# Performance work log

Measured on AMD Instinct MI355X. Metric: run time of the kernel, lower is better.

## Reference

```python
import jax, jax.numpy as jnp
import numpy as np

EPS = 1e-8
TEMP = 0.1
D, H = 512, 256  # hidden_dim, hidden_dim // 2
BI, R = 64, 36   # images, regions
BC, W = 64, 50   # captions, words


def _l2norm(x):
    n = jnp.linalg.norm(x, axis=-1, keepdims=True)
    return x / jnp.maximum(n, 1e-12)


def _gate(x, w1, b1, w2, b2):
    h = jax.nn.relu(x @ w1 + b1)
    return jax.nn.sigmoid(h @ w2 + b2)  # [..., 1]


def setup_inputs() -> dict:
    key = jax.random.key(0)
    ks = jax.random.split(key, 12)
    imgs = jax.random.normal(ks[0], (BI, R, D), dtype=jnp.float32)
    caps = jax.random.normal(ks[1], (BC, W, D), dtype=jnp.float32)
    img_lens = jax.random.randint(ks[2], (BI,), 1, R + 1).at[0].set(R).astype(jnp.int32)
    cap_lens = jax.random.randint(ks[3], (BC,), 1, W + 1).at[0].set(W).astype(jnp.int32)
    s = 0.02
    return {
        'imgs': imgs, 'caps': caps,
        'soft_w1': jax.random.normal(ks[4], (D, H), dtype=jnp.float32) * s,
        'soft_b1': jnp.zeros((H,), dtype=jnp.float32),
        'soft_w2': jax.random.normal(ks[5], (H, 1), dtype=jnp.float32) * s,
        'soft_b2': jnp.zeros((1,), dtype=jnp.float32),
        'hard_w1': jax.random.normal(ks[6], (D, H), dtype=jnp.float32) * s,
        'hard_b1': jnp.zeros((H,), dtype=jnp.float32),
        'hard_w2': jax.random.normal(ks[7], (H, 1), dtype=jnp.float32) * s,
        'hard_b2': jnp.zeros((1,), dtype=jnp.float32),
        'img_lens': img_lens, 'cap_lens': cap_lens,
    }


def reference(imgs, caps, soft_w1, soft_b1, soft_w2, soft_b2,
              hard_w1, hard_b1, hard_w2, hard_b2, img_lens, cap_lens):
    Bi, R_, D_ = imgs.shape
    Bc, W_, _ = caps.shape
    img_mask = jnp.arange(R_)[None, :] < img_lens[:, None]  # [Bi,R]
    cap_mask = jnp.arange(W_)[None, :] < cap_lens[:, None]  # [Bc,W]
    mask = img_mask[:, None, :, None] & cap_mask[None, :, None, :]  # [Bi,Bc,R,W]

    # fine-grained region-word similarities
    sims = jnp.einsum('ird,cwd->icrw', imgs, caps)

    # hard (top-1) attention: argmax over words, one-hot scatter, re-masked
    idx = jnp.argmax(jnp.where(mask, sims, -1.0), axis=-1)  # [Bi,Bc,R]
    hard_attn = jnp.where(mask, jax.nn.one_hot(idx, W_, dtype=sims.dtype), 0.0)

    # soft attention with temperature and mask
    soft = jax.nn.softmax(jnp.where(mask, sims / TEMP, -jnp.inf), axis=-1)
    soft_attn = jnp.where(mask, soft, 0.0)

    hard_wc = jnp.einsum('icrw,cwd->icrd', hard_attn, caps)
    soft_wc = jnp.einsum('icrw,cwd->icrd', soft_attn, caps)

    # per-region learned gates, normalized to sum ~1
    sg = _gate(imgs, soft_w1, soft_b1, soft_w2, soft_b2)  # [Bi,R,1]
    hg = _gate(imgs, hard_w1, hard_b1, hard_w2, hard_b2)  # [Bi,R,1]
    tot = sg + hg + EPS
    sg = (sg / tot)[:, None, :, :]  # [Bi,1,R,1]
    hg = (hg / tot)[:, None, :, :]

    mixed = sg * soft_wc + hg * hard_wc  # [Bi,Bc,R,D]

    # per-pair, per-region cosine similarity
    out = jnp.einsum('ird,icrd->icr', _l2norm(imgs), _l2norm(mixed))
    return jnp.where(img_mask[:, None, :], out, -1.0)  # [Bi,Bc,R]
```

## Files before the change

kernel.cpp:

```cpp
#include <hip/hip_runtime.h>
#include <math.h>

#define BI 64
#define RR 36
#define BC 64
#define WW 50
#define DD 512
#define HH 256
#define CST 132

typedef _Float16 f16x8 __attribute__((ext_vector_type(8)));
typedef _Float16 f16x4 __attribute__((ext_vector_type(4)));
typedef float    f32x4 __attribute__((ext_vector_type(4)));
typedef float    f32x16 __attribute__((ext_vector_type(16)));

__device__ __forceinline__ float wave_sum(float v){
  #pragma unroll
  for (int off=32; off>0; off>>=1) v += __shfl_xor(v, off, 64);
  return v;
}
__device__ __forceinline__ float wave_max(float v){
  #pragma unroll
  for (int off=32; off>0; off>>=1) v = fmaxf(v, __shfl_xor(v, off, 64));
  return v;
}

__device__ __forceinline__ void gl_lds16(const _Float16* g, _Float16* l){
  __builtin_amdgcn_global_load_lds(
      (const __attribute__((address_space(1))) unsigned int*)g,
      (__attribute__((address_space(3))) unsigned int*)l, 16, 0, 0);
}

__global__ __launch_bounds__(256) void prepgram_kernel(
    const float* __restrict__ imgs, const float* __restrict__ caps,
    const float* __restrict__ sw1, const float* __restrict__ hw1,
    _Float16* __restrict__ Ah, _Float16* __restrict__ Al,
    _Float16* __restrict__ Bh, _Float16* __restrict__ Bl,
    float* __restrict__ G, _Float16* __restrict__ Gfrag)
{
  __shared__ __align__(16) float smem[64*64];
  if (blockIdx.x < 1504){
    int u = blockIdx.x*256 + threadIdx.x;
    _Float16 *dh, *dl; int idx;
    if (u < 144*1024){ idx = u;            dh = Ah; dl = Al; }
    else             { idx = u - 144*1024; dh = Bh; dl = Bl; }
    const int tile = idx >> 10, rem = idx & 1023, ks = rem >> 6, lane = rem & 63;
    const int k0 = ks*32 + (lane >> 4)*8;
    f16x8 hv, lv;
    if (u < 144*1024 || tile < 200){
      const float* src = (u < 144*1024) ? imgs : caps;
      const int m = tile*16 + (lane & 15);
      const float* p = src + (size_t)m*DD + k0;
      #pragma unroll
      for (int j=0;j<8;j++){
        float a = p[j];
        _Float16 h = (_Float16)a;
        hv[j] = h;
        lv[j] = (_Float16)((a - (float)h) * 2048.0f);
      }
    } else {
      const int n = (tile-200)*16 + (lane & 15);
      const float* src = (n < HH) ? (sw1 + n) : (hw1 + n - HH);
      #pragma unroll
      for (int j=0;j<8;j++){
        float a = src[(size_t)(k0+j)*HH];
        _Float16 h = (_Float16)a;
        hv[j] = h;
        lv[j] = (_Float16)((a - (float)h) * 2048.0f);
      }
    }
    *(f16x8*)(dh + (size_t)idx*8) = hv;
    *(f16x8*)(dl + (size_t)idx*8) = lv;
  } else {
    float* Gt = smem;
    const int c = blockIdx.x - 1504;
    const int t = threadIdx.x, lane = t & 63, wv = t >> 6;
    const int wm = wv & 1, wn = wv >> 1;
    const float* cbase = caps + (size_t)c*WW*DD;

    f32x16 P, Q;
    #pragma unroll
    for (int e=0;e<16;e++){ P[e]=0.f; Q[e]=0.f; }

    const int r  = lane & 31;
    const int k8 = (lane >> 5)*8;
    const int wA = wm*32 + r;
    const int wB = wn*32 + r;
    const float* pA = cbase + (size_t)wA*DD + k8;
    const float* pB = cbase + (size_t)wB*DD + k8;

    for (int ks=0; ks<32; ks++){
      const int k0 = ks*16;
      float4 a0, a1, b0, b1;
      if (wA < WW){ a0 = *(const float4*)(pA + k0); a1 = *(const float4*)(pA + k0 + 4); }
      else        { a0 = (float4){0,0,0,0}; a1 = a0; }
      if (wB < WW){ b0 = *(const float4*)(pB + k0); b1 = *(const float4*)(pB + k0 + 4); }
      else        { b0 = (float4){0,0,0,0}; b1 = b0; }
      float av[8] = {a0.x,a0.y,a0.z,a0.w,a1.x,a1.y,a1.z,a1.w};
      float bw[8] = {b0.x,b0.y,b0.z,b0.w,b1.x,b1.y,b1.z,b1.w};
      f16x8 ah, al, bh, bl;
      #pragma unroll
      for (int j=0;j<8;j++){
        _Float16 h = (_Float16)av[j];
        ah[j] = h; al[j] = (_Float16)((av[j]-(float)h)*2048.0f);
        _Float16 g = (_Float16)bw[j];
        bh[j] = g; bl[j] = (_Float16)((bw[j]-(float)g)*2048.0f);
      }
      P = __builtin_amdgcn_mfma_f32_32x32x16_f16(ah, bh, P,0,0,0);
      Q = __builtin_amdgcn_mfma_f32_32x32x16_f16(ah, bl, Q,0,0,0);
      Q = __builtin_amdgcn_mfma_f32_32x32x16_f16(al, bh, Q,0,0,0);
    }

    const int col = wn*32 + (lane & 31);
    #pragma unroll
    for (int reg=0; reg<16; reg++){
      const int row = wm*32 + (reg&3) + 8*(reg>>2) + 4*(lane>>5);
      float g = P[reg] + Q[reg]*(1.0f/2048.0f);
      Gt[row*64 + col] = g;
      if (row < WW && col < WW)
        G[(size_t)c*WW*WW + row*WW + col] = g;
    }
    __syncthreads();

    #pragma unroll
    for (int tile=0; tile<4; tile++){
      int flat = t*4;
      int ks2 = flat>>9, L=(flat>>3)&63, j0=flat&7;
      const bool ones = (tile==3) && ((L&15)==2);
      int n  = tile*16 + (L&15);
      int kk = ks2*32 + ((L>>4)<<3) + j0;
      f16x4 v;
      #pragma unroll
      for (int e=0;e<4;e++)
        v[e] = ones ? (_Float16)1.0f : (_Float16)Gt[n*64 + kk + e];
      *(f16x4*)&Gfrag[(size_t)c*4096 + (tile*2+ks2)*512 + L*8 + j0] = v;
    }
  }
}

__global__ __launch_bounds__(256, 2) void sgemm_hgate_kernel(
    const _Float16* __restrict__ Ah, const _Float16* __restrict__ Al,
    const _Float16* __restrict__ Bh, const _Float16* __restrict__ Bl,
    float* __restrict__ Sp,
    const float* __restrict__ imgs,
    const float* __restrict__ sb1, const float* __restrict__ hb1,
    const float* __restrict__ sw2, const float* __restrict__ hw2,
    float* __restrict__ drawS, float* __restrict__ drawH,
    float* __restrict__ rnraw)
{
  __shared__ _Float16 lds[2*16384];
  const int t = threadIdx.x, lane = t & 63, wv = t >> 6;

  if (blockIdx.x >= 36){
    const int sg  = blockIdx.x - 36;
    const int xcd = sg & 7, sidx = sg >> 3;
    const int l   = (xcd < 2 ? xcd*57 : 114 + (xcd-2)*56) + sidx;
    const int st  = l / 45, wi = l - st*45;
    const int mbg = st & 1, nbg = st >> 1;
    const int mb  = mbg*9 + wi/5;
    const int nb  = nbg*5 + wi%5;
    const int wm = wv & 1, wn = wv >> 1;

    f32x4 P[4][4], Q[4][4];
    #pragma unroll
    for (int a=0;a<4;a++)
      #pragma unroll
      for (int b=0;b<4;b++){ P[a][b]=(f32x4){0,0,0,0}; Q[a][b]=(f32x4){0,0,0,0}; }

    const _Float16* sbase = (wv==0)?Ah:(wv==1)?Al:(wv==2)?Bh:Bl;
    const size_t gtb = (size_t)((wv<2)? mb : nb)*8;
    _Float16* buf0 = lds + wv*4096;
    _Float16* buf1 = lds + 16384 + wv*4096;

    #pragma unroll
    for (int s=0;s<8;s++)
      gl_lds16(sbase + (((gtb+s)*16 + 0)*64 + lane)*8, buf0 + s*512);
    asm volatile("s_waitcnt vmcnt(0)" ::: "memory");
    __syncthreads();

    for (int ks=0; ks<16; ks++){
      if (ks < 15){
        _Float16* nb_ = ((ks+1) & 1) ? buf1 : buf0;
        #pragma unroll
        for (int s=0;s<8;s++)
          gl_lds16(sbase + (((gtb+s)*16 + (ks+1))*64 + lane)*8, nb_ + s*512);
      }

      const _Float16* L = lds + (ks & 1)*16384;
      f16x8 a_h[4], a_l[4], b_h[4], b_l[4];
      #pragma unroll
      for (int x=0;x<4;x++){
        a_h[x] = *(const f16x8*)&L[        (wm*4+x)*512 + lane*8];
        a_l[x] = *(const f16x8*)&L[ 4096 + (wm*4+x)*512 + lane*8];
        b_h[x] = *(const f16x8*)&L[ 8192 + (wn*4+x)*512 + lane*8];
        b_l[x] = *(const f16x8*)&L[12288 + (wn*4+x)*512 + lane*8];
      }
      #pragma unroll
      for (int mi=0;mi<4;mi++)
        #pragma unroll
        for (int ni=0;ni<4;ni++){
          P[mi][ni] = __builtin_amdgcn_mfma_f32_16x16x32_f16(a_h[mi], b_h[ni], P[mi][ni],0,0,0);
          Q[mi][ni] = __builtin_amdgcn_mfma_f32_16x16x32_f16(a_h[mi], b_l[ni], Q[mi][ni],0,0,0);
          Q[mi][ni] = __builtin_amdgcn_mfma_f32_16x16x32_f16(a_l[mi], b_h[ni], Q[mi][ni],0,0,0);
        }

      if (ks < 15)
        asm volatile("s_waitcnt vmcnt(0)" ::: "memory");
      __syncthreads();
    }

    const int r0 = mb*128 + wm*64 + ((lane>>4)<<2);
    const int c0 = nb*128 + wn*64 + (lane&15);
    size_t pr[16]; size_t pc[4];
    #pragma unroll
    for (int mi=0;mi<4;mi++)
      #pragma unroll
      for (int reg=0;reg<4;reg++){
        unsigned row = (unsigned)(r0 + mi*16 + reg);
        unsigned i = row / 36u, rr_ = row - i*36u;
        pr[mi*4+reg] = (size_t)i*115200u + (size_t)rr_*50u;
      }
    #pragma unroll
    for (int ni=0;ni<4;ni++){
      unsigned col = (unsigned)(c0 + ni*16);
      unsigned cc = col / 50u, w = col - cc*50u;
      pc[ni] = (size_t)cc*1800u + w;
    }
    #pragma unroll
    for (int mi=0;mi<4;mi++)
      #pragma unroll
      for (int ni=0;ni<4;ni++)
        #pragma unroll
        for (int reg=0;reg<4;reg++)
          Sp[pr[mi*4+reg] + pc[ni]] =
              P[mi][ni][reg] + Q[mi][ni][reg]*(1.0f/2048.0f);
    return;
  }

  const int mb = blockIdx.x >> 1;
  const int br = blockIdx.x & 1;
  const int wm = wv & 1, wn = wv >> 1;

  f32x4 P[4][8];
  #pragma unroll
  for (int a=0;a<4;a++)
    #pragma unroll
    for (int b=0;b<8;b++) P[a][b]=(f32x4){0,0,0,0};

  const _Float16* Bbase = Bh + (size_t)(200 + br*16)*8192;

  #pragma unroll
  for (int s=0;s<6;s++){
    const int u = wv*6 + s;
    const _Float16* src = (u < 8)
      ? (Ah    + ((size_t)((mb*8 + u)*16 + 0)*64 + lane)*8)
      : (Bbase + ((size_t)((u-8)  *16 + 0)*64 + lane)*8);
    _Float16* dst = (u < 8) ? (lds + u*512) : (lds + 4096 + (u-8)*512);
    gl_lds16(src, dst);
  }
  asm volatile("s_waitcnt vmcnt(0)" ::: "memory");
  __syncthreads();

  for (int ks=0; ks<16; ks++){
    if (ks < 15){
      _Float16* buf = lds + (((ks+1) & 1) ? 16384 : 0);
      #pragma unroll
      for (int s=0;s<6;s++){
        const int u = wv*6 + s;
        const _Float16* src = (u < 8)
          ? (Ah    + ((size_t)((mb*8 + u)*16 + (ks+1))*64 + lane)*8)
          : (Bbase + ((size_t)((u-8)  *16 + (ks+1))*64 + lane)*8);
        _Float16* dst = (u < 8) ? (buf + u*512) : (buf + 4096 + (u-8)*512);
        gl_lds16(src, dst);
      }
    }

    const _Float16* L = lds + (ks & 1)*16384;
    f16x8 a[4], b[8];
    #pragma unroll
    for (int x=0;x<4;x++)
      a[x] = *(const f16x8*)&L[(wm*4+x)*512 + lane*8];
    #pragma unroll
    for (int y=0;y<8;y++)
      b[y] = *(const f16x8*)&L[4096 + (wn*8+y)*512 + lane*8];
    #pragma unroll
    for (int mi=0;mi<4;mi++)
      #pragma unroll
      for (int ni=0;ni<8;ni++)
        P[mi][ni] = __builtin_amdgcn_mfma_f32_16x16x32_f16(a[mi], b[ni], P[mi][ni],0,0,0);

    if (ks < 15)
      asm volatile("s_waitcnt vmcnt(0)" ::: "memory");
    __syncthreads();
  }

  const float* b1 = br ? hb1 : sb1;
  const float* w2 = br ? hw2 : sw2;
  float bvv[8], wvv[8];
  #pragma unroll
  for (int ni=0;ni<8;ni++){
    const int cb = wn*128 + ni*16 + (lane&15);
    bvv[ni] = b1[cb]; wvv[ni] = w2[cb];
  }
  float contrib[16];
  #pragma unroll
  for (int mi=0;mi<4;mi++)
    #pragma unroll
    for (int reg=0;reg<4;reg++){
      float cacc = 0.f;
      #pragma unroll
      for (int ni=0;ni<8;ni++)
        cacc = fmaf(fmaxf(P[mi][ni][reg] + bvv[ni], 0.f), wvv[ni], cacc);
      #pragma unroll
      for (int off=1; off<16; off<<=1) cacc += __shfl_xor(cacc, off, 64);
      contrib[mi*4+reg] = cacc;
    }

  float* red = (float*)lds;
  if ((lane & 15) == 0){
    const int rbase = wm*64 + ((lane>>4)<<2);
    #pragma unroll
    for (int mi=0;mi<4;mi++)
      #pragma unroll
      for (int reg=0;reg<4;reg++)
        red[wn*128 + rbase + mi*16 + reg] = contrib[mi*4+reg];
  }
  __syncthreads();
  if (t < 128){
    float draw = red[t] + red[128 + t];
    (br ? drawH : drawS)[mb*128 + t] = draw;
  }

  if (br == 0){
    const int row = mb*128 + (t >> 1);
    const float* p = imgs + (size_t)row*DD + (t & 1)*256;
    float ss = 0.f;
    #pragma unroll
    for (int q=0;q<64;q++){
      float4 x = ((const float4*)p)[q];
      ss += x.x*x.x + x.y*x.y + x.z*x.z + x.w*x.w;
    }
    ss += __shfl_xor(ss, 1, 64);
    if ((t & 1) == 0) rnraw[row] = ss;
  }
}

__global__ __launch_bounds__(512) void epi_kernel(
    const float* __restrict__ Sp,
    const int* __restrict__ img_lens, const int* __restrict__ cap_lens,
    const float* __restrict__ drawS, const float* __restrict__ drawH,
    const float* __restrict__ rnraw,
    const float* __restrict__ G, const _Float16* __restrict__ Gfrag,
    const float* __restrict__ sb2, const float* __restrict__ hb2,
    float* __restrict__ out)
{
  __shared__ __align__(16) _Float16 sEp[48*72];
  __shared__ __align__(16) _Float16 sE2[48*72];
  __shared__ __align__(16) _Float16 sFp[48*72];
  __shared__ __align__(16) _Float16 sGf[4096];
  __shared__ float sTd[48];
  __shared__ float sTS[48];
  __shared__ float sGd[64];
  __shared__ float sAv[40];
  __shared__ int   sAi[40];

  const int bx = blockIdx.x;
  const int i = bx >> 6, c = bx & 63;
  const int t = threadIdx.x, lane = t & 63;
  const int wv = __builtin_amdgcn_readfirstlane(t >> 6);
  const int cap_len = cap_lens[c];
  const int img_len = img_lens[i];

  ((int4*)sGf)[t] = ((const int4*)(Gfrag + (size_t)c*4096))[t];
  if (t < WW) sGd[t] = G[(size_t)c*WW*WW + t*(WW+1)];

  const int r0 = wv*5;
  const float* srow = Sp + (size_t)(i*64 + c)*1800u + (size_t)r0*50;
  float sv[5];
  #pragma unroll
  for (int j=0;j<5;j++)
    sv[j] = ((r0+j) < RR && lane < WW) ? srow[j*50 + lane] : 0.f;

  #pragma unroll
  for (int j=0;j<5;j++){
    const int r = r0 + j;
    const float s = sv[j];
    const bool valid = (lane < cap_len);
    float av = wave_max(valid ? s : -INFINITY);
    unsigned long long m = __ballot(valid && (s == av));
    int ai = (int)(__ffsll((long long)m) - 1);
    float e = valid ? __expf(10.0f*(s - av)) : 0.f;
    sEp[r*72 + lane] = (_Float16)e;
    sE2[r*72 + lane] = (_Float16)(e * s);
    if (lane == 0){ sAv[r] = av; sAi[r] = ai; }
  }
  __syncthreads();

  {
    int mi = wv % 3, nt = wv / 3;
    f32x4 acc = (f32x4){0,0,0,0};
    #pragma unroll
    for (int ks=0; ks<2; ks++){
      f16x8 a = *(const f16x8*)&sEp[(mi*16+(lane&15))*72 + ks*32 + ((lane>>4)<<3)];
      f16x8 b = *(const f16x8*)&sGf[(nt*2+ks)*512 + lane*8];
      acc = __builtin_amdgcn_mfma_f32_16x16x32_f16(a, b, acc, 0,0,0);
    }
    #pragma unroll
    for (int reg=0; reg<4; reg++){
      int row = mi*16 + ((lane>>4)<<2) + reg;
      sFp[row*72 + nt*16 + (lane&15)] = (_Float16)acc[reg];
    }
  }
  if (wv < 4){
    int tau = 8 + wv, mi = tau % 3, nt = tau / 3;
    f32x4 acc = (f32x4){0,0,0,0};
    #pragma unroll
    for (int ks=0; ks<2; ks++){
      f16x8 a = *(const f16x8*)&sEp[(mi*16+(lane&15))*72 + ks*32 + ((lane>>4)<<3)];
      f16x8 b = *(const f16x8*)&sGf[(nt*2+ks)*512 + lane*8];
      acc = __builtin_amdgcn_mfma_f32_16x16x32_f16(a, b, acc, 0,0,0);
    }
    #pragma unroll
    for (int reg=0; reg<4; reg++){
      int row = mi*16 + ((lane>>4)<<2) + reg;
      sFp[row*72 + nt*16 + (lane&15)] = (_Float16)acc[reg];
    }
  } else if (wv < 7){
    int mi = wv - 4;
    f32x4 acc = (f32x4){0,0,0,0};
    #pragma unroll
    for (int ks=0; ks<2; ks++){
      f16x8 a = *(const f16x8*)&sE2[(mi*16+(lane&15))*72 + ks*32 + ((lane>>4)<<3)];
      f16x8 b = *(const f16x8*)&sGf[(3*2+ks)*512 + lane*8];
      acc = __builtin_amdgcn_mfma_f32_16x16x32_f16(a, b, acc, 0,0,0);
    }
    if ((lane & 15) == 2){
      #pragma unroll
      for (int reg=0; reg<4; reg++)
        sTS[mi*16 + ((lane>>4)<<2) + reg] = acc[reg];
    }
  }
  __syncthreads();

  if (wv < 3){
    f32x4 acc = (f32x4){0,0,0,0};
    #pragma unroll
    for (int ks=0; ks<2; ks++){
      f16x8 aF = *(const f16x8*)&sFp[(wv*16+(lane&15))*72 + ks*32 + ((lane>>4)<<3)];
      f16x8 bE = *(const f16x8*)&sEp[(wv*16+(lane&15))*72 + ks*32 + ((lane>>4)<<3)];
      acc = __builtin_amdgcn_mfma_f32_16x16x32_f16(aF, bE, acc, 0,0,0);
    }
    #pragma unroll
    for (int reg=0; reg<4; reg++){
      int row = ((lane>>4)<<2) + reg;
      if (row == (lane&15)) sTd[wv*16 + row] = acc[reg];
    }
  }
  __syncthreads();

  if (wv == 0 && lane < RR){
    const int r = lane;
    const int ai = sAi[r];
    const float av = sAv[r];
    float tQ  = sTd[r];
    float tS  = sTS[r];
    float den = (float)sFp[r*72 + 50];
    float dh  = (float)sFp[r*72 + ai];
    float hh  = sGd[ai];
    float hv  = (av > -1.0f) ? 1.f : 0.f;

    const int rg = i*RR + r;
    float sg_ = 1.f/(1.f+__expf(-(drawS[rg] + sb2[0])));
    float hg_ = 1.f/(1.f+__expf(-(drawH[rg] + hb2[0])));
    float tot = sg_ + hg_ + 1e-8f;
    float gs = sg_/tot, gh = hg_/tot;
    float rx = 1.f/fmaxf(sqrtf(rnraw[rg]), 1e-12f);
    float rd = 1.f/den;
    float num = gs*(tS*rd) + hv*gh*av;
    float n2  = gs*gs*(tQ*rd*rd) + hv*(2.f*gs*gh*(dh*rd) + gh*gh*hh);
    float ov  = num * rx / fmaxf(sqrtf(fmaxf(n2, 0.f)), 1e-12f);
    out[((size_t)i*BC + c)*RR + r] = (r < img_len) ? ov : -1.0f;
  }
}

__global__ __launch_bounds__(256) void gates_kernel(
    const float* __restrict__ imgs,
    const float* __restrict__ sw1, const float* __restrict__ sb1,
    const float* __restrict__ sw2, const float* __restrict__ sb2,
    const float* __restrict__ hw1, const float* __restrict__ hb1,
    const float* __restrict__ hw2, const float* __restrict__ hb2,
    float* __restrict__ sgn, float* __restrict__ hgn, float* __restrict__ rn)
{
  __shared__ __align__(16) float xs[8*DD];
  __shared__ float red[16*256];
  __shared__ float nr[8];
  const int t = threadIdx.x;
  const int row0 = blockIdx.x * 8;
  if (t < 8) nr[t] = 0.f;
  __syncthreads();
  const float4* src = (const float4*)(imgs + (size_t)row0*DD);
  #pragma unroll
  for (int m=0;m<4;m++){
    int n = m*256+t;
    float4 v = src[n];
    ((float4*)xs)[n] = v;
    float ss = v.x*v.x+v.y*v.y+v.z*v.z+v.w*v.w;
    atomicAdd(&nr[n>>7], ss);
  }
  __syncthreads();
  float accS[8]={0,0,0,0,0,0,0,0};
  float accH[8]={0,0,0,0,0,0,0,0};
  for (int k=0;k<DD;k+=4){
    float a0=sw1[(k+0)*HH+t], a1=sw1[(k+1)*HH+t], a2=sw1[(k+2)*HH+t], a3=sw1[(k+3)*HH+t];
    float b0=hw1[(k+0)*HH+t], b1=hw1[(k+1)*HH+t], b2=hw1[(k+2)*HH+t], b3=hw1[(k+3)*HH+t];
    #pragma unroll
    for (int r=0;r<8;r++){
      float4 x = *(const float4*)&xs[r*DD+k];
      accS[r]=fmaf(x.x,a0,accS[r]); accS[r]=fmaf(x.y,a1,accS[r]);
      accS[r]=fmaf(x.z,a2,accS[r]); accS[r]=fmaf(x.w,a3,accS[r]);
      accH[r]=fmaf(x.x,b0,accH[r]); accH[r]=fmaf(x.y,b1,accH[r]);
      accH[r]=fmaf(x.z,b2,accH[r]); accH[r]=fmaf(x.w,b3,accH[r]);
    }
  }
  const float b1s=sb1[t], b1h=hb1[t], w2s=sw2[t], w2h=hw2[t];
  #pragma unroll
  for (int r=0;r<8;r++){
    red[r*256+t]     = w2s * fmaxf(accS[r]+b1s, 0.f);
    red[(8+r)*256+t] = w2h * fmaxf(accH[r]+b1h, 0.f);
  }
  __syncthreads();
  const int wv=t>>6, ln=t&63;
  #pragma unroll
  for (int q=0;q<4;q++){
    int rr_ = wv*4+q;
    float v = red[rr_*256+ln]+red[rr_*256+ln+64]+red[rr_*256+ln+128]+red[rr_*256+ln+192];
    v = wave_sum(v);
    if (ln==0) red[rr_*256] = v;
  }
  __syncthreads();
  if (t<8){
    float os = red[t*256] + sb2[0];
    float oh = red[(8+t)*256] + hb2[0];
    float s = 1.f/(1.f+__expf(-os));
    float h = 1.f/(1.f+__expf(-oh));
    float tot = s+h+1e-8f;
    sgn[row0+t] = s/tot;
    hgn[row0+t] = h/tot;
    rn[row0+t]  = 1.f/fmaxf(sqrtf(nr[t]), 1e-12f);
  }
}

__global__ __launch_bounds__(256) void gram_fb_kernel(
    const float* __restrict__ caps, float* __restrict__ G)
{
  __shared__ __align__(16) float cs[WW*CST];
  const int c    = blockIdx.x >> 2;
  const int tile = blockIdx.x & 3;
  const int w0   = tile*13;
  const int nw   = (tile==3) ? 11 : 13;
  const int t=threadIdx.x, lane=t&63, wv=t>>6;
  const int wl = lane < WW ? lane : WW-1;
  float acc[4]={0.f,0.f,0.f,0.f};
  for (int k0=0;k0<DD;k0+=128){
    __syncthreads();
    for (int n=t;n<WW*32;n+=256){
      int row=n>>5, c4=(n&31)*4;
      *(float4*)&cs[row*CST+c4] = *(const float4*)(caps + ((size_t)c*WW+row)*DD + k0 + c4);
    }
    __syncthreads();
    for (int k=0;k<128;k+=4){
      float4 cv = *(const float4*)&cs[wl*CST+k];
      #pragma unroll
      for (int q=0;q<4;q++){
        int lw = wv + q*4;
        if (lw < nw){
          float4 bv = *(const float4*)&cs[(w0+lw)*CST+k];
          acc[q]=fmaf(bv.x,cv.x,acc[q]); acc[q]=fmaf(bv.y,cv.y,acc[q]);
          acc[q]=fmaf(bv.z,cv.z,acc[q]); acc[q]=fmaf(bv.w,cv.w,acc[q]);
        }
      }
    }
  }
  if (lane < WW){
    #pragma unroll
    for (int q=0;q<4;q++){
      int lw = wv + q*4;
      if (lw < nw) G[(size_t)c*WW*WW + (w0+lw)*WW + lane] = acc[q];
    }
  }
}

__global__ __launch_bounds__(256) void pair_kernel(
    const float* __restrict__ imgs, const float* __restrict__ caps,
    const int* __restrict__ img_lens, const int* __restrict__ cap_lens,
    const float* __restrict__ sgn, const float* __restrict__ hgn,
    const float* __restrict__ rn,
    const float* __restrict__ G, float* __restrict__ out)
{
  __shared__ __align__(16) float smem[WW*CST + 52*52 + RR*52];
  float* cs = smem;
  float* Gs = smem + WW*CST;
  float* As = Gs + 52*52;
  const int bx = blockIdx.x;
  const int i = bx >> 6, c = bx & 63;
  const int t = threadIdx.x, lane = t&63;
  const int wv = __builtin_amdgcn_readfirstlane(t>>6);
  const int wl = lane < WW ? lane : WW-1;
  const int cap_len = cap_lens[c];
  const int img_len = img_lens[i];
  for (int n=t;n<52*52;n+=256){
    int w=n/52, w2=n-w*52;
    Gs[n] = (w<WW && w2<WW) ? G[(size_t)c*WW*WW + w*WW + w2] : 0.f;
  }
  float acc[9]={0,0,0,0,0,0,0,0,0};
  const float* ib = imgs + ((size_t)i*RR + wv*9)*DD;
  for (int k0=0;k0<DD;k0+=128){
    __syncthreads();
    for (int n=t;n<WW*32;n+=256){
      int row=n>>5, c4=(n&31)*4;
      *(float4*)&cs[row*CST+c4] = *(const float4*)(caps + ((size_t)c*WW+row)*DD + k0 + c4);
    }
    __syncthreads();
    for (int k=0;k<128;k+=4){
      float4 cv = *(const float4*)&cs[wl*CST+k];
      #pragma unroll
      for (int j=0;j<9;j++){
        float4 iv = *(const float4*)(ib + j*DD + k0 + k);
        acc[j]=fmaf(iv.x,cv.x,acc[j]); acc[j]=fmaf(iv.y,cv.y,acc[j]);
        acc[j]=fmaf(iv.z,cv.z,acc[j]); acc[j]=fmaf(iv.w,cv.w,acc[j]);
      }
    }
  }
  for (int j=0;j<9;j++){
    const int r = wv*9 + j;
    const float s = acc[j];
    float av; int ai;
    if (lane < cap_len){ av = s;     ai = lane; }
    else if (lane < WW){ av = -1.0f; ai = lane; }
    else               { av = -INFINITY; ai = 64; }
    #pragma unroll
    for (int off=32; off>0; off>>=1){
      float ov = __shfl_xor(av, off, 64);
      int   oi = __shfl_xor(ai, off, 64);
      if (ov > av || (ov == av && oi < ai)){ av = ov; ai = oi; }
    }
    float zv = (lane < cap_len) ? s*10.0f : -INFINITY;
    float zm = wave_max(zv);
    float e  = (lane < cap_len) ? __expf(zv - zm) : 0.f;
    float den = wave_sum(e);
    if (lane < 52) As[r*52 + lane] = (lane < WW) ? e : 0.f;
    float m = 0.f;
    #pragma unroll
    for (int g=0; g<13; g++){
      float4 ab = *(const float4*)&As[r*52 + g*4];
      m = fmaf(ab.x, Gs[(g*4+0)*52+wl], m);
      m = fmaf(ab.y, Gs[(g*4+1)*52+wl], m);
      m = fmaf(ab.z, Gs[(g*4+2)*52+wl], m);
      m = fmaf(ab.w, Gs[(g*4+3)*52+wl], m);
    }
    float tS = wave_sum(e * s);
    float tQ = wave_sum(e * m);
    float dh = __shfl(m, ai, 64);
    float hh = Gs[ai*52 + ai];
    float hv = (ai < cap_len) ? 1.f : 0.f;
    const int rg = i*RR + r;
    float gs = sgn[rg], gh = hgn[rg], rx = rn[rg];
    float rd = 1.f/den;
    float num = gs*(tS*rd) + hv*gh*av;
    float n2  = gs*gs*(tQ*rd*rd) + hv*(2.f*gs*gh*(dh*rd) + gh*gh*hh);
    float ov  = num * rx / fmaxf(sqrtf(fmaxf(n2, 0.f)), 1e-12f);
    if (lane==0) out[((size_t)i*BC + c)*RR + r] = (r < img_len) ? ov : -1.0f;
  }
}

extern "C" void kernel_launch(void* const* d_in, const int* in_sizes, int n_in,
                              void* d_out, int out_size, void* d_ws, size_t ws_size,
                              hipStream_t stream)
{
  const float* imgs = (const float*)d_in[0];
  const float* caps = (const float*)d_in[1];
  const float* sw1  = (const float*)d_in[2];
  const float* sb1  = (const float*)d_in[3];
  const float* sw2  = (const float*)d_in[4];
  const float* sb2  = (const float*)d_in[5];
  const float* hw1  = (const float*)d_in[6];
  const float* hb1  = (const float*)d_in[7];
  const float* hw2  = (const float*)d_in[8];
  const float* hb2  = (const float*)d_in[9];
  const int* img_lens = (const int*)d_in[10];
  const int* cap_lens = (const int*)d_in[11];

  char* base = (char*)d_ws;
  float*    drawS = (float*)(base + 0);
  float*    drawH = (float*)(base + 9216);
  float*    rnraw = (float*)(base + 18432);
  float*    G     = (float*)(base + 27648);
  _Float16* Gfrag = (_Float16*)(base + 667648);
  _Float16* Ah    = (_Float16*)(base + 1191936);
  _Float16* Al    = (_Float16*)(base + 3551232);
  _Float16* Bh    = (_Float16*)(base + 5910528);
  _Float16* Bl    = (_Float16*)(base + 9711616);
  float*    Sp    = (float*)(base + 18231296);
  const size_t NEED = 47722496ull;

  float* out = (float*)d_out;

  if (ws_size >= NEED){
    hipLaunchKernelGGL(prepgram_kernel, dim3(1568), dim3(256), 0, stream,
                       imgs, caps, sw1, hw1, Ah, Al, Bh, Bl, G, Gfrag);
    hipLaunchKernelGGL(sgemm_hgate_kernel, dim3(486), dim3(256), 0, stream,
                       Ah, Al, Bh, Bl, Sp,
                       imgs, sb1, hb1, sw2, hw2, drawS, drawH, rnraw);
    hipLaunchKernelGGL(epi_kernel, dim3(BI*BC), dim3(512), 0, stream,
                       Sp, img_lens, cap_lens, drawS, drawH, rnraw,
                       G, Gfrag, sb2, hb2, out);
  } else {
    hipLaunchKernelGGL(gates_kernel, dim3(288), dim3(256), 0, stream,
                       imgs, sw1, sb1, sw2, sb2, hw1, hb1, hw2, hb2,
                       drawS, drawH, rnraw);
    hipLaunchKernelGGL(gram_fb_kernel, dim3(256), dim3(256), 0, stream, caps, G);
    hipLaunchKernelGGL(pair_kernel, dim3(BI*BC), dim3(256), 0, stream,
                       imgs, caps, img_lens, cap_lens, drawS, drawH, rnraw, G, out);
  }
}
```

Before: 152.6 us.

## Restructure epilogue to one wave per image-caption pair with register-held fragments

The epilogue kernel now assigns one wavefront per (image, caption) pair, four pairs per 256-thread block, instead of a 512-thread block per pair. Similarity rows are loaded straight into MFMA operand layout in registers. Argmax, softmax denominators and the e*s sums are computed with in-register reductions, and the E·G product and the quadratic term use per-wave LDS scratch, which removes most block-level syncs and shared staging. The cost is higher register pressure and slightly different fp16 rounding order in the denominator and the tS/tQ terms. The workspace size requirement is also bumped.

```diff
diff --git a/kernel.cpp b/kernel.cpp
--- a/kernel.cpp
+++ b/kernel.cpp
@@ -345,7 +345,7 @@
   }
 }
 
-__global__ __launch_bounds__(512) void epi_kernel(
+__global__ __launch_bounds__(256) void epi_kernel(
     const float* __restrict__ Sp,
     const int* __restrict__ img_lens, const int* __restrict__ cap_lens,
     const float* __restrict__ drawS, const float* __restrict__ drawH,
@@ -354,132 +354,131 @@
     const float* __restrict__ sb2, const float* __restrict__ hb2,
     float* __restrict__ out)
 {
-  __shared__ __align__(16) _Float16 sEp[48*72];
-  __shared__ __align__(16) _Float16 sE2[48*72];
-  __shared__ __align__(16) _Float16 sFp[48*72];
-  __shared__ __align__(16) _Float16 sGf[4096];
-  __shared__ float sTd[48];
-  __shared__ float sTS[48];
-  __shared__ float sGd[64];
-  __shared__ float sAv[40];
-  __shared__ int   sAi[40];
-
-  const int bx = blockIdx.x;
-  const int i = bx >> 6, c = bx & 63;
+  __shared__ __align__(16) _Float16 FT[4][48*72];
   const int t = threadIdx.x, lane = t & 63;
   const int wv = __builtin_amdgcn_readfirstlane(t >> 6);
+  const int pair = blockIdx.x*4 + wv;
+  const int i = pair >> 6, c = pair & 63;
+  const int l = lane & 15, g = lane >> 4;
   const int cap_len = cap_lens[c];
   const int img_len = img_lens[i];
 
-  ((int4*)sGf)[t] = ((const int4*)(Gfrag + (size_t)c*4096))[t];
-  if (t < WW) sGd[t] = G[(size_t)c*WW*WW + t*(WW+1)];
-
-  const int r0 = wv*5;
-  const float* srow = Sp + (size_t)(i*64 + c)*1800u + (size_t)r0*50;
-  float sv[5];
-  #pragma unroll
-  for (int j=0;j<5;j++)
-    sv[j] = ((r0+j) < RR && lane < WW) ? srow[j*50 + lane] : 0.f;
-
-  #pragma unroll
-  for (int j=0;j<5;j++){
-    const int r = r0 + j;
-    const float s = sv[j];
-    const bool valid = (lane < cap_len);
-    float av = wave_max(valid ? s : -INFINITY);
-    unsigned long long m = __ballot(valid && (s == av));
-    int ai = (int)(__ffsll((long long)m) - 1);
-    float e = valid ? __expf(10.0f*(s - av)) : 0.f;
-    sEp[r*72 + lane] = (_Float16)e;
-    sE2[r*72 + lane] = (_Float16)(e * s);
-    if (lane == 0){ sAv[r] = av; sAi[r] = ai; }
-  }
-  __syncthreads();
-
-  {
-    int mi = wv % 3, nt = wv / 3;
-    f32x4 acc = (f32x4){0,0,0,0};
-    #pragma unroll
-    for (int ks=0; ks<2; ks++){
-      f16x8 a = *(const f16x8*)&sEp[(mi*16+(lane&15))*72 + ks*32 + ((lane>>4)<<3)];
-      f16x8 b = *(const f16x8*)&sGf[(nt*2+ks)*512 + lane*8];
-      acc = __builtin_amdgcn_mfma_f32_16x16x32_f16(a, b, acc, 0,0,0);
-    }
-    #pragma unroll
-    for (int reg=0; reg<4; reg++){
-      int row = mi*16 + ((lane>>4)<<2) + reg;
-      sFp[row*72 + nt*16 + (lane&15)] = (_Float16)acc[reg];
-    }
-  }
-  if (wv < 4){
-    int tau = 8 + wv, mi = tau % 3, nt = tau / 3;
-    f32x4 acc = (f32x4){0,0,0,0};
-    #pragma unroll
-    for (int ks=0; ks<2; ks++){
-      f16x8 a = *(const f16x8*)&sEp[(mi*16+(lane&15))*72 + ks*32 + ((lane>>4)<<3)];
-      f16x8 b = *(const f16x8*)&sGf[(nt*2+ks)*512 + lane*8];
-      acc = __builtin_amdgcn_mfma_f32_16x16x32_f16(a, b, acc, 0,0,0);
-    }
-    #pragma unroll
-    for (int reg=0; reg<4; reg++){
-      int row = mi*16 + ((lane>>4)<<2) + reg;
-      sFp[row*72 + nt*16 + (lane&15)] = (_Float16)acc[reg];
-    }
-  } else if (wv < 7){
-    int mi = wv - 4;
-    f32x4 acc = (f32x4){0,0,0,0};
-    #pragma unroll
-    for (int ks=0; ks<2; ks++){
-      f16x8 a = *(const f16x8*)&sE2[(mi*16+(lane&15))*72 + ks*32 + ((lane>>4)<<3)];
-      f16x8 b = *(const f16x8*)&sGf[(3*2+ks)*512 + lane*8];
-      acc = __builtin_amdgcn_mfma_f32_16x16x32_f16(a, b, acc, 0,0,0);
-    }
-    if ((lane & 15) == 2){
-      #pragma unroll
-      for (int reg=0; reg<4; reg++)
-        sTS[mi*16 + ((lane>>4)<<2) + reg] = acc[reg];
-    }
-  }
-  __syncthreads();
-
-  if (wv < 3){
-    f32x4 acc = (f32x4){0,0,0,0};
-    #pragma unroll
-    for (int ks=0; ks<2; ks++){
-      f16x8 aF = *(const f16x8*)&sFp[(wv*16+(lane&15))*72 + ks*32 + ((lane>>4)<<3)];
-      f16x8 bE = *(const f16x8*)&sEp[(wv*16+(lane&15))*72 + ks*32 + ((lane>>4)<<3)];
-      acc = __builtin_amdgcn_mfma_f32_16x16x32_f16(aF, bE, acc, 0,0,0);
-    }
-    #pragma unroll
-    for (int reg=0; reg<4; reg++){
-      int row = ((lane>>4)<<2) + reg;
-      if (row == (lane&15)) sTd[wv*16 + row] = acc[reg];
-    }
-  }
-  __syncthreads();
-
-  if (wv == 0 && lane < RR){
-    const int r = lane;
-    const int ai = sAi[r];
-    const float av = sAv[r];
-    float tQ  = sTd[r];
-    float tS  = sTS[r];
-    float den = (float)sFp[r*72 + 50];
-    float dh  = (float)sFp[r*72 + ai];
-    float hh  = sGd[ai];
-    float hv  = (av > -1.0f) ? 1.f : 0.f;
-
-    const int rg = i*RR + r;
-    float sg_ = 1.f/(1.f+__expf(-(drawS[rg] + sb2[0])));
-    float hg_ = 1.f/(1.f+__expf(-(drawH[rg] + hb2[0])));
-    float tot = sg_ + hg_ + 1e-8f;
-    float gs = sg_/tot, gh = hg_/tot;
-    float rx = 1.f/fmaxf(sqrtf(rnraw[rg]), 1e-12f);
-    float rd = 1.f/den;
-    float num = gs*(tS*rd) + hv*gh*av;
-    float n2  = gs*gs*(tQ*rd*rd) + hv*(2.f*gs*gh*(dh*rd) + gh*gh*hh);
-    float ov  = num * rx / fmaxf(sqrtf(fmaxf(n2, 0.f)), 1e-12f);
-    out[((size_t)i*BC + c)*RR + r] = (r < img_len) ? ov : -1.0f;
+  int4 gf[8];
+  #pragma unroll
+  for (int q=0;q<8;q++)
+    gf[q] = ((const int4*)(Gfrag + (size_t)c*4096))[q*64 + lane];
+
+  const float* sbp = Sp + (size_t)i*115200 + (size_t)c*1800;
+  float sv[3][16];
+  #pragma unroll
+  for (int nt=0;nt<3;nt++)
+    #pragma unroll
+    for (int ks=0;ks<2;ks++){
+      const float* p = sbp + (nt*16+l)*50 + ks*32 + g*8;
+      #pragma unroll
+      for (int h=0;h<4;h++){
+        float2 v2 = *(const float2*)(p + h*2);
+        sv[nt][ks*8 + h*2]     = v2.x;
+        sv[nt][ks*8 + h*2 + 1] = v2.y;
+      }
+    }
+
+  float avA[3]; int aiA[3]; float denA[3], tSA[3];
+  f16x8 e16[3][2];
+  #pragma unroll
+  for (int nt=0;nt<3;nt++){
+    float best = -INFINITY; int bw = 64;
+    #pragma unroll
+    for (int j=0;j<16;j++){
+      int w = (j>>3)*32 + g*8 + (j&7);
+      if (w < cap_len){
+        float s = sv[nt][j];
+        if (s > best){ best = s; bw = w; }
+      }
+    }
+    #pragma unroll
+    for (int off=16; off<64; off<<=1){
+      float ov = __shfl_xor(best, off, 64);
+      int   ow = __shfl_xor(bw,   off, 64);
+      if (ov > best || (ov == best && ow < bw)){ best = ov; bw = ow; }
+    }
+    avA[nt] = best; aiA[nt] = (bw < 64) ? bw : 0;
+
+    float dsum = 0.f, tsum = 0.f;
+    #pragma unroll
+    for (int ks=0;ks<2;ks++)
+      #pragma unroll
+      for (int j=0;j<8;j++){
+        int w = ks*32 + g*8 + j;
+        float s = sv[nt][ks*8+j];
+        float e = (w < cap_len) ? __expf(10.0f*(s - best)) : 0.f;
+        _Float16 eh = (_Float16)e;
+        e16[nt][ks][j] = eh;
+        dsum += (float)eh;
+        tsum += (float)(_Float16)(e * s);
+      }
+    dsum += __shfl_xor(dsum,16,64); dsum += __shfl_xor(dsum,32,64);
+    tsum += __shfl_xor(tsum,16,64); tsum += __shfl_xor(tsum,32,64);
+    denA[nt] = dsum; tSA[nt] = tsum;
+  }
+
+  _Float16* ft = &FT[wv][0];
+  #pragma unroll
+  for (int mt=0;mt<4;mt++)
+    #pragma unroll
+    for (int nt=0;nt<3;nt++){
+      f32x4 acc = (f32x4){0,0,0,0};
+      #pragma unroll
+      for (int ks=0;ks<2;ks++){
+        f16x8 ga = *(const f16x8*)&gf[mt*2+ks];
+        acc = __builtin_amdgcn_mfma_f32_16x16x32_f16(ga, e16[nt][ks], acc,0,0,0);
+      }
+      f16x4 fv;
+      #pragma unroll
+      for (int r2=0;r2<4;r2++) fv[r2] = (_Float16)acc[r2];
+      *(f16x4*)&ft[(nt*16+l)*72 + mt*16 + g*4] = fv;
+    }
+
+  float tQA[3];
+  #pragma unroll
+  for (int nt=0;nt<3;nt++){
+    float q = 0.f;
+    #pragma unroll
+    for (int ks=0;ks<2;ks++){
+      f16x8 fv = *(const f16x8*)&ft[(nt*16+l)*72 + ks*32 + g*8];
+      #pragma unroll
+      for (int j=0;j<8;j++)
+        q += (float)e16[nt][ks][j] * (float)fv[j];
+    }
+    q += __shfl_xor(q,16,64); q += __shfl_xor(q,32,64);
+    tQA[nt] = q;
+  }
+
+  if (lane < 16){
+    const float sb2v = sb2[0], hb2v = hb2[0];
+    #pragma unroll
+    for (int nt=0;nt<3;nt++){
+      const int rr = nt*16 + lane;
+      if (rr < RR){
+        const int ai = aiA[nt];
+        const float av = avA[nt];
+        float dh = (float)ft[rr*72 + ai];
+        float hh = G[(size_t)c*WW*WW + ai*(WW+1)];
+        float hv = (av > -1.0f) ? 1.f : 0.f;
+        const int rg = i*RR + rr;
+        float sg_ = 1.f/(1.f+__expf(-(drawS[rg] + sb2v)));
+        float hg_ = 1.f/(1.f+__expf(-(drawH[rg] + hb2v)));
+        float tot = sg_ + hg_ + 1e-8f;
+        float gs = sg_/tot, gh = hg_/tot;
+        float rx = 1.f/fmaxf(sqrtf(rnraw[rg]), 1e-12f);
+        float dn = (float)(_Float16)denA[nt];
+        float rd = 1.f/dn;
+        float num = gs*(tSA[nt]*rd) + hv*gh*av;
+        float n2  = gs*gs*(tQA[nt]*rd*rd) + hv*(2.f*gs*gh*(dh*rd) + gh*gh*hh);
+        float ov  = num * rx / fmaxf(sqrtf(fmaxf(n2, 0.f)), 1e-12f);
+        out[((size_t)i*BC + c)*RR + rr] = (rr < img_len) ? ov : -1.0f;
+      }
+    }
   }
 }
 
@@ -701,7 +700,7 @@
   _Float16* Bh    = (_Float16*)(base + 5910528);
   _Float16* Bl    = (_Float16*)(base + 9711616);
   float*    Sp    = (float*)(base + 18231296);
-  const size_t NEED = 47722496ull;
+  const size_t NEED = 47726592ull;
 
   float* out = (float*)d_out;
 
@@ -711,7 +710,7 @@
     hipLaunchKernelGGL(sgemm_hgate_kernel, dim3(486), dim3(256), 0, stream,
                        Ah, Al, Bh, Bl, Sp,
                        imgs, sb1, hb1, sw2, hw2, drawS, drawH, rnraw);
-    hipLaunchKernelGGL(epi_kernel, dim3(BI*BC), dim3(512), 0, stream,
+    hipLaunchKernelGGL(epi_kernel, dim3(1024), dim3(256), 0, stream,
                        Sp, img_lens, cap_lens, drawS, drawH, rnraw,
                        G, Gfrag, sb2, hb2, out);
   } else {
```

After: 142.7 us (median of 2 runs). 1.07x faster.
